# Kernel optimization log

Hardware: AMD Instinct MI355X
Metric: run time of the kernel (lower is better)

## Reference

```python
import jax, jax.numpy as jnp
import numpy as np

D_MODEL = 1024
N_HEAD = 16
D_K = D_MODEL // N_HEAD
NEG = -1000000000.0


def setup_inputs() -> dict:
    key = jax.random.key(0)
    ks = jax.random.split(key, 12)
    B, S = 4, 2048
    scale = 1.0 / np.sqrt(D_MODEL)
    inp = {
        "q": jax.random.normal(ks[0], (B, S, D_MODEL), jnp.float32),
        "k": jax.random.normal(ks[1], (B, S, D_MODEL), jnp.float32),
        "v": jax.random.normal(ks[2], (B, S, D_MODEL), jnp.float32),
        "mask": jnp.ones((1, 1, S, S), jnp.int32),
        "w_Q": jax.random.normal(ks[3], (D_MODEL, D_MODEL), jnp.float32) * scale,
        "b_Q": jnp.zeros((D_MODEL,), jnp.float32),
        "w_K": jax.random.normal(ks[4], (D_MODEL, D_MODEL), jnp.float32) * scale,
        "b_K": jnp.zeros((D_MODEL,), jnp.float32),
        "w_V": jax.random.normal(ks[5], (D_MODEL, D_MODEL), jnp.float32) * scale,
        "b_V": jnp.zeros((D_MODEL,), jnp.float32),
        "w_O": jax.random.normal(ks[6], (D_MODEL, D_MODEL), jnp.float32) * scale,
        "b_O": jnp.zeros((D_MODEL,), jnp.float32),
    }
    return inp


def reference(q, k, v, mask, w_Q, b_Q, w_K, b_K, w_V, b_V, w_O, b_O):
    B, S, _ = q.shape
    # linear projections (torch Linear: x @ W^T + b)
    qp = q @ w_Q.T + b_Q
    kp = k @ w_K.T + b_K
    vp = v @ w_V.T + b_V
    # [B,S,D] -> [B,H,S,d_k]
    qh = qp.reshape(B, S, N_HEAD, D_K).transpose(0, 2, 1, 3)
    kh = kp.reshape(B, S, N_HEAD, D_K).transpose(0, 2, 1, 3)
    vh = vp.reshape(B, S, N_HEAD, D_K).transpose(0, 2, 1, 3)
    # scores [B,H,S,S]
    scores = jnp.einsum("bhqd,bhkd->bhqk", qh, kh) / jnp.sqrt(jnp.float32(D_K))
    scores = jnp.where(mask == 0, jnp.float32(NEG), scores)
    attn = jax.nn.softmax(scores, axis=-1)  # dropout p=0.0 -> identity
    ctx = jnp.einsum("bhqk,bhkd->bhqd", attn, vh)
    ctx = ctx.transpose(0, 2, 1, 3).reshape(B, S, D_MODEL)
    return ctx @ w_O.T + b_O
```

## Files before the change

### kernel.cpp

```cpp
#include <hip/hip_runtime.h>
#include <hip/hip_bf16.h>
#include <cmath>

#define D_MODEL 1024
#define N_HEAD 16
#define D_K 64

typedef __attribute__((ext_vector_type(8))) short short8;
typedef __attribute__((ext_vector_type(4))) float f32x4;
typedef __attribute__((ext_vector_type(16))) float f32x16;

#define GL_LDS16(gp, lp)                                                                   \
  __builtin_amdgcn_global_load_lds((const __attribute__((address_space(1))) unsigned int*)(gp), \
                                   (__attribute__((address_space(3))) unsigned int*)(lp), 16, 0, 0)

#if __has_builtin(__builtin_amdgcn_exp2f)
#define EXP2(x) __builtin_amdgcn_exp2f(x)
#else
#define EXP2(x) exp2f(x)
#endif

__device__ __forceinline__ unsigned short f2bu(float x) {
  __hip_bfloat16 h = __float2bfloat16(x);
  return *reinterpret_cast<unsigned short*>(&h);
}

__device__ __forceinline__ unsigned int cvtpk(float lo, float hi) {
  unsigned int r;
  asm("v_cvt_pk_bf16_f32 %0, %1, %2" : "=v"(r) : "v"(lo), "v"(hi));
  return r;
}

__device__ __forceinline__ float max3f(float a, float b, float c) {
  return fmaxf(fmaxf(a, b), c);
}

__device__ __forceinline__ void plswap(unsigned int& a, unsigned int& b) {
#if __has_builtin(__builtin_amdgcn_permlane32_swap)
  auto r = __builtin_amdgcn_permlane32_swap((int)a, (int)b, false, false);
  a = (unsigned int)r[0];
  b = (unsigned int)r[1];
#else
  unsigned int ax = (unsigned int)__shfl_xor((int)a, 32);
  unsigned int bx = (unsigned int)__shfl_xor((int)b, 32);
  bool hi = (threadIdx.x & 32) != 0;
  unsigned int na = hi ? bx : a;
  unsigned int nb = hi ? b : ax;
  a = na; b = nb;
#endif
}

__global__ __launch_bounds__(256) void f2b3_kernel(const float* __restrict__ a, const float* __restrict__ b,
                                                   const float* __restrict__ c,
                                                   unsigned short* __restrict__ oa, unsigned short* __restrict__ ob,
                                                   unsigned short* __restrict__ oc, int n) {
  const float* src = (blockIdx.y == 0) ? a : (blockIdx.y == 1) ? b : c;
  unsigned short* dst = (blockIdx.y == 0) ? oa : (blockIdx.y == 1) ? ob : oc;
  int i = (blockIdx.x * 256 + threadIdx.x) * 4;
  if (i >= n) return;
  float4 v = *reinterpret_cast<const float4*>(src + i);
  ushort4 o;
  o.x = f2bu(v.x); o.y = f2bu(v.y); o.z = f2bu(v.z); o.w = f2bu(v.w);
  *reinterpret_cast<ushort4*>(dst + i) = o;
}

__global__ __launch_bounds__(256) void f2b4_kernel(const float* __restrict__ a, const float* __restrict__ b,
                                                   const float* __restrict__ c, const float* __restrict__ d,
                                                   unsigned short* __restrict__ oa, unsigned short* __restrict__ ob,
                                                   unsigned short* __restrict__ oc, unsigned short* __restrict__ od,
                                                   int n) {
  const float* src = (blockIdx.y == 0) ? a : (blockIdx.y == 1) ? b : (blockIdx.y == 2) ? c : d;
  unsigned short* dst = (blockIdx.y == 0) ? oa : (blockIdx.y == 1) ? ob : (blockIdx.y == 2) ? oc : od;
  int i = (blockIdx.x * 256 + threadIdx.x) * 4;
  if (i >= n) return;
  float4 v = *reinterpret_cast<const float4*>(src + i);
  ushort4 o;
  o.x = f2bu(v.x); o.y = f2bu(v.y); o.z = f2bu(v.z); o.w = f2bu(v.w);
  *reinterpret_cast<ushort4*>(dst + i) = o;
}

template <int OUTF32>
__global__ __launch_bounds__(256) void gemm_bt_kernel(
    const unsigned short* __restrict__ A0, const unsigned short* __restrict__ A1,
    const unsigned short* __restrict__ A2,
    const unsigned short* __restrict__ W0, const unsigned short* __restrict__ W1,
    const unsigned short* __restrict__ W2,
    const float* __restrict__ b0, const float* __restrict__ b1, const float* __restrict__ b2,
    void* __restrict__ Cout, int Msub, int N, int K,
    float s0, float s1, float s2) {
  __shared__ __align__(16) unsigned short lA[2][128 * 64];
  __shared__ __align__(16) unsigned short lB[2][128 * 64];

  const int tid = threadIdx.x;
  const int lane = tid & 63;
  const int w = tid >> 6;
  const int wm = w >> 1, wn = w & 1;
  const int lr = lane & 15, lg = lane >> 4;
  const int wavebase = tid & ~63;

  int m0g, n0;
  {
    const int nbx = gridDim.x;
    const int nb = nbx * gridDim.y;
    int lin = blockIdx.y * nbx + blockIdx.x;
    int wid = lin;
    if ((nb & 7) == 0) wid = (lin & 7) * (nb >> 3) + (lin >> 3);
    n0 = (wid % nbx) * 128;
    m0g = (wid / nbx) * 128;
  }
  const int mtile = m0g >> 7;
  const int which = mtile / (Msub >> 7);
  const int m0 = m0g - which * Msub;
  const unsigned short* A  = (which == 0) ? A0 : (which == 1) ? A1 : A2;
  const unsigned short* Bw = (which == 0) ? W0 : (which == 1) ? W1 : W2;
  const float* bias = (which == 0) ? b0 : (which == 1) ? b1 : b2;
  const float oscale = (which == 0) ? s0 : (which == 1) ? s1 : s2;

  f32x4 acc[4][4] = {};

  auto stage = [&](int buf, int k0) {
#pragma unroll
    for (int j = 0; j < 4; ++j) {
      int chunk = j * 256 + tid;
      int row = chunk >> 3, cc = chunk & 7;
      GL_LDS16(A + (size_t)(m0 + row) * K + k0 + cc * 8,
               (char*)&lA[buf][0] + (j * 256 + wavebase) * 16);
    }
#pragma unroll
    for (int j = 0; j < 4; ++j) {
      int chunk = j * 256 + tid;
      int row = chunk >> 3, cc = chunk & 7;
      GL_LDS16(Bw + (size_t)(n0 + row) * K + k0 + cc * 8,
               (char*)&lB[buf][0] + (j * 256 + wavebase) * 16);
    }
  };

  stage(0, 0);
  const int nk = K / 64;
  for (int t = 0; t < nk; ++t) {
    const int buf = t & 1;
    __syncthreads();
    if (t + 1 < nk) stage(buf ^ 1, (t + 1) * 64);
#pragma unroll
    for (int kk = 0; kk < 2; ++kk) {
      short8 a[4], bfr[4];
#pragma unroll
      for (int m = 0; m < 4; ++m)
        a[m] = *reinterpret_cast<const short8*>(
            &lA[buf][(wm * 64 + m * 16 + lr) * 64 + kk * 32 + lg * 8]);
#pragma unroll
      for (int n = 0; n < 4; ++n)
        bfr[n] = *reinterpret_cast<const short8*>(
            &lB[buf][(wn * 64 + n * 16 + lr) * 64 + kk * 32 + lg * 8]);
#pragma unroll
      for (int m = 0; m < 4; ++m)
#pragma unroll
        for (int n = 0; n < 4; ++n)
          acc[m][n] = __builtin_amdgcn_mfma_f32_16x16x32_bf16(a[m], bfr[n], acc[m][n], 0, 0, 0);
    }
  }

#pragma unroll
  for (int n = 0; n < 4; ++n) {
    const int gc = n0 + wn * 64 + n * 16 + lr;
    const float bn = bias[gc];
#pragma unroll
    for (int m = 0; m < 4; ++m) {
      const int gr0 = m0g + wm * 64 + m * 16 + lg * 4;
#pragma unroll
      for (int i = 0; i < 4; ++i) {
        float v = (acc[m][n][i] + bn) * oscale;
        if (OUTF32)
          reinterpret_cast<float*>(Cout)[(size_t)(gr0 + i) * N + gc] = v;
        else
          reinterpret_cast<unsigned short*>(Cout)[(size_t)(gr0 + i) * N + gc] = f2bu(v);
      }
    }
  }
}

__global__ __launch_bounds__(512, 4) void attn_kernel(
    const unsigned short* __restrict__ Qp, const unsigned short* __restrict__ Kp,
    const unsigned short* __restrict__ Vp, unsigned short* __restrict__ Ctx, int S) {
  __shared__ __align__(16) unsigned short Ks[2][64 * 64];
  __shared__ __align__(16) unsigned short Vt[2][64 * 64];

  const int tid = threadIdx.x;
  const int lane = tid & 63;
  const int wv = tid >> 6;
  const int l31 = lane & 31;
  const int hf = lane >> 5;

  const int nqb = gridDim.x;
  const int total = nqb * gridDim.y;
  int f = blockIdx.y * nqb + blockIdx.x;
  int g = ((total & 7) == 0) ? ((f & 7) * (total >> 3) + (f >> 3)) : f;
  const int bh = g / nqb;
  const int b = bh >> 4;
  const int head = bh & 15;
  const int q0 = (g % nqb) * 256;
  const int qrow = q0 + wv * 32 + l31;

  int av[4], av2[4];
#pragma unroll
  for (int c = 0; c < 4; ++c) {
    int chunk = ((c * 2 + hf) ^ (l31 & 7) ^ (l31 >> 3)) & 7;
    av[c] = l31 * 128 + (chunk << 4);
    av2[c] = (av[c] ^ 0x40) + 4096;
  }

  const unsigned short* qptr = Qp + (size_t)(b * S + qrow) * D_MODEL + head * 64;
  short8 qf[4];
#pragma unroll
  for (int ds = 0; ds < 4; ++ds)
    qf[ds] = *reinterpret_cast<const short8*>(qptr + ds * 16 + hf * 8);

  const int t256 = tid & 255;
  const int dblk = t256 & 15, kblk = t256 >> 4;
  const int dv0 = dblk * 4, key0 = kblk * 4;
  int wbyte[4];
#pragma unroll
  for (int j = 0; j < 4; ++j) {
    int row = dv0 + j;
    int slot = ((key0 >> 3) ^ (row & 7) ^ ((row >> 3) & 7)) & 7;
    wbyte[j] = row * 128 + (slot << 4) + ((key0 & 4) << 1);
  }

  float m_run = -1e30f, l_run = 0.0f;
  f32x16 oacc0 = {}, oacc1 = {};

  auto stageK = [&](int buf, int t) {
    const size_t baseK = (size_t)(b * S + t * 64) * D_MODEL + head * 64;
#pragma unroll
    for (int j = 0; j < 2; ++j) {
      int c = j * 256 + t256;
      int r = c >> 3, w8 = c & 7;
      int w8s = w8 ^ (r & 7) ^ ((r >> 3) & 7);
      GL_LDS16(Kp + baseK + (size_t)r * D_MODEL + w8s * 8,
               (char*)&Ks[buf][0] + (j * 256 + (t256 & ~63)) * 16);
    }
  };

  uint2 vr0, vr1, vr2, vr3;
  auto loadV = [&](int t) {
    const unsigned short* vptr =
        Vp + (size_t)(b * S + t * 64 + key0) * D_MODEL + head * 64 + dv0;
    vr0 = *reinterpret_cast<const uint2*>(vptr);
    vr1 = *reinterpret_cast<const uint2*>(vptr + D_MODEL);
    vr2 = *reinterpret_cast<const uint2*>(vptr + 2 * D_MODEL);
    vr3 = *reinterpret_cast<const uint2*>(vptr + 3 * D_MODEL);
  };

  if (wv >= 4) stageK(0, 0);
  else loadV(0);

  const int nt = S / 64;
  auto tile = [&](const int buf, const int t) {
    if (wv < 4) {
      char* vb = (char*)&Vt[buf][0];
      unsigned int o0x = __builtin_amdgcn_perm(vr1.x, vr0.x, 0x05040100u);
      unsigned int o0y = __builtin_amdgcn_perm(vr3.x, vr2.x, 0x05040100u);
      unsigned int o1x = __builtin_amdgcn_perm(vr1.x, vr0.x, 0x07060302u);
      unsigned int o1y = __builtin_amdgcn_perm(vr3.x, vr2.x, 0x07060302u);
      unsigned int o2x = __builtin_amdgcn_perm(vr1.y, vr0.y, 0x05040100u);
      unsigned int o2y = __builtin_amdgcn_perm(vr3.y, vr2.y, 0x05040100u);
      unsigned int o3x = __builtin_amdgcn_perm(vr1.y, vr0.y, 0x07060302u);
      unsigned int o3y = __builtin_amdgcn_perm(vr3.y, vr2.y, 0x07060302u);
      *reinterpret_cast<uint2*>(vb + wbyte[0]) = make_uint2(o0x, o0y);
      *reinterpret_cast<uint2*>(vb + wbyte[1]) = make_uint2(o1x, o1y);
      *reinterpret_cast<uint2*>(vb + wbyte[2]) = make_uint2(o2x, o2y);
      *reinterpret_cast<uint2*>(vb + wbyte[3]) = make_uint2(o3x, o3y);
    }
    __syncthreads();
    if (t + 1 < nt) {
      if (wv >= 4) stageK(buf ^ 1, t + 1);
      else loadV(t + 1);
    }

    const char* kbp = (const char*)&Ks[buf][0];
    const char* vbp = (const char*)&Vt[buf][0];

#pragma unroll
    for (int h2 = 0; h2 < 2; ++h2) {
      f32x16 sacc = {};
      __builtin_amdgcn_s_setprio(1);
#pragma unroll
      for (int ds = 0; ds < 4; ++ds) {
        short8 a0 = *reinterpret_cast<const short8*>(kbp + (h2 ? av2[ds] : av[ds]));
        sacc = __builtin_amdgcn_mfma_f32_32x32x16_bf16(a0, qf[ds], sacc, 0, 0, 0);
      }
      __builtin_amdgcn_s_setprio(0);

      float a0 = max3f(sacc[0], sacc[1], sacc[2]);
      float a1 = max3f(sacc[3], sacc[4], sacc[5]);
      float a2 = max3f(sacc[6], sacc[7], sacc[8]);
      float a3 = max3f(sacc[9], sacc[10], sacc[11]);
      float a4 = max3f(sacc[12], sacc[13], sacc[14]);
      float b0 = max3f(a0, a1, sacc[15]);
      float b1 = max3f(a2, a3, a4);
      float rmax_h = fmaxf(b0, b1);
      float rmax = fmaxf(rmax_h, __shfl_xor(rmax_h, 32));

      if (__any(rmax > m_run + 8.0f)) {
        float mnew = fmaxf(m_run, rmax);
        float al = EXP2(m_run - mnew);
        m_run = mnew;
        l_run *= al;
#pragma unroll
        for (int r = 0; r < 16; ++r) { oacc0[r] *= al; oacc1[r] *= al; }
      }

#pragma unroll
      for (int r = 0; r < 16; ++r) sacc[r] = EXP2(sacc[r] - m_run);

      float s0 = (sacc[0] + sacc[1]) + (sacc[2] + sacc[3]);
      float s1 = (sacc[4] + sacc[5]) + (sacc[6] + sacc[7]);
      float s2 = (sacc[8] + sacc[9]) + (sacc[10] + sacc[11]);
      float s3 = (sacc[12] + sacc[13]) + (sacc[14] + sacc[15]);
      float rsum = (s0 + s1) + (s2 + s3);
      rsum += __shfl_xor(rsum, 32);
      l_run += rsum;

      unsigned int W[8];
#pragma unroll
      for (int m = 0; m < 8; ++m) W[m] = cvtpk(sacc[2 * m], sacc[2 * m + 1]);
      short8 pf[2];
#pragma unroll
      for (int s = 0; s < 2; ++s) {
        unsigned int u0 = W[4 * s + 0], u2 = W[4 * s + 2];
        unsigned int u1 = W[4 * s + 1], u3 = W[4 * s + 3];
        plswap(u0, u2); plswap(u1, u3);
        int4 wvv = make_int4((int)u0, (int)u1, (int)u2, (int)u3);
        pf[s] = *reinterpret_cast<short8*>(&wvv);
      }

      __builtin_amdgcn_s_setprio(1);
#pragma unroll
      for (int s = 0; s < 2; ++s) {
        short8 va = *reinterpret_cast<const short8*>(vbp + av[h2 * 2 + s]);
        oacc0 = __builtin_amdgcn_mfma_f32_32x32x16_bf16(va, pf[s], oacc0, 0, 0, 0);
        short8 vb2 = *reinterpret_cast<const short8*>(vbp + av2[h2 * 2 + s]);
        oacc1 = __builtin_amdgcn_mfma_f32_32x32x16_bf16(vb2, pf[s], oacc1, 0, 0, 0);
      }
      __builtin_amdgcn_s_setprio(0);
    }
  };

  for (int t = 0; t < nt; t += 2) {
    tile(0, t);
    tile(1, t + 1);
  }

  const float linv = 1.0f / l_run;
  unsigned short* cp = Ctx + (size_t)(b * S + qrow) * D_MODEL + head * 64;
#pragma unroll
  for (int g2 = 0; g2 < 4; ++g2) {
    ushort4 o;
    o.x = f2bu(oacc0[4 * g2 + 0] * linv);
    o.y = f2bu(oacc0[4 * g2 + 1] * linv);
    o.z = f2bu(oacc0[4 * g2 + 2] * linv);
    o.w = f2bu(oacc0[4 * g2 + 3] * linv);
    *reinterpret_cast<ushort4*>(cp + 8 * g2 + 4 * hf) = o;
    ushort4 o2;
    o2.x = f2bu(oacc1[4 * g2 + 0] * linv);
    o2.y = f2bu(oacc1[4 * g2 + 1] * linv);
    o2.z = f2bu(oacc1[4 * g2 + 2] * linv);
    o2.w = f2bu(oacc1[4 * g2 + 3] * linv);
    *reinterpret_cast<ushort4*>(cp + 32 + 8 * g2 + 4 * hf) = o2;
  }
}

extern "C" void kernel_launch(void* const* d_in, const int* in_sizes, int n_in,
                              void* d_out, int out_size, void* d_ws, size_t ws_size,
                              hipStream_t stream) {
  const float* q  = (const float*)d_in[0];
  const float* k  = (const float*)d_in[1];
  const float* v  = (const float*)d_in[2];
  const float* wQ = (const float*)d_in[4];
  const float* bQ = (const float*)d_in[5];
  const float* wK = (const float*)d_in[6];
  const float* bK = (const float*)d_in[7];
  const float* wV = (const float*)d_in[8];
  const float* bV = (const float*)d_in[9];
  const float* wO = (const float*)d_in[10];
  const float* bO = (const float*)d_in[11];
  float* out = (float*)d_out;

  int S = 1;
  while ((long)S * S < (long)in_sizes[3]) S <<= 1;
  const int Bn = in_sizes[0] / (S * D_MODEL);
  const int M = Bn * S;

  unsigned short* xq   = (unsigned short*)d_ws;
  unsigned short* wqb  = xq + (size_t)M * D_MODEL;
  unsigned short* wkb  = wqb + (size_t)D_MODEL * D_MODEL;
  unsigned short* wvb  = wkb + (size_t)D_MODEL * D_MODEL;
  unsigned short* wob  = wvb + (size_t)D_MODEL * D_MODEL;
  unsigned short* qkvp = wob + (size_t)D_MODEL * D_MODEL;
  unsigned short* qp = qkvp;
  unsigned short* kp = qkvp + (size_t)M * D_MODEL;
  unsigned short* vp = qkvp + 2 * (size_t)M * D_MODEL;
  unsigned short* xk = (unsigned short*)d_out;
  unsigned short* xv = xk + (size_t)M * D_MODEL;

  const int DW = D_MODEL * D_MODEL;
  f2b4_kernel<<<dim3(DW / 1024, 4), 256, 0, stream>>>(wQ, wK, wV, wO, wqb, wkb, wvb, wob, DW);

  const int NX = M * D_MODEL;
  f2b3_kernel<<<dim3(NX / 1024, 3), 256, 0, stream>>>(q, k, v, xq, xk, xv, NX);

  const float qscale = 0.125f * 1.4426950408889634f;

  gemm_bt_kernel<0><<<dim3(D_MODEL / 128, 3 * M / 128), 256, 0, stream>>>(
      xq, xk, xv, wqb, wkb, wvb, bQ, bK, bV, qkvp, M, D_MODEL, D_MODEL,
      qscale, 1.0f, 1.0f);

  attn_kernel<<<dim3(S / 256, Bn * N_HEAD), 512, 0, stream>>>(qp, kp, vp, xq, S);

  gemm_bt_kernel<1><<<dim3(D_MODEL / 128, M / 128), 256, 0, stream>>>(
      xq, xq, xq, wob, wob, wob, bO, bO, bO, out, M, D_MODEL, D_MODEL,
      1.0f, 1.0f, 1.0f);
}
```

Before: 222.1 us.

## Triple-buffer projection GEMM with swizzled LDS and explicit vmcnt waits

The projection GEMM moves from a double-buffered K=64 tile to a triple-buffered K=32 tile. LDS chunks are XOR-swizzled to avoid bank conflicts on the MFMA fragment reads. Explicit s_waitcnt vmcnt counts and raw barriers let up to two future stages stay in flight, and s_setprio is raised around the MFMA block. This aims to hide global-to-LDS latency and cut LDS conflicts, at the cost of more barriers per K step and hand-tuned wait counts that must match the number of loads issued per stage.

```diff
diff --git a/kernel.cpp b/kernel.cpp
--- a/kernel.cpp
+++ b/kernel.cpp
@@ -88,8 +88,8 @@
     const float* __restrict__ b0, const float* __restrict__ b1, const float* __restrict__ b2,
     void* __restrict__ Cout, int Msub, int N, int K,
     float s0, float s1, float s2) {
-  __shared__ __align__(16) unsigned short lA[2][128 * 64];
-  __shared__ __align__(16) unsigned short lB[2][128 * 64];
+  __shared__ __align__(16) unsigned short lA[3][128 * 32];
+  __shared__ __align__(16) unsigned short lB[3][128 * 32];
 
   const int tid = threadIdx.x;
   const int lane = tid & 63;
@@ -118,46 +118,66 @@
 
   f32x4 acc[4][4] = {};
 
+  const int swz = (lg ^ (lr & 3) ^ ((lr >> 2) & 3)) << 4;
+  int avA[4], avB[4];
+#pragma unroll
+  for (int m = 0; m < 4; ++m) {
+    avA[m] = (wm * 64 + m * 16 + lr) * 64 + swz;
+    avB[m] = (wn * 64 + m * 16 + lr) * 64 + swz;
+  }
+
   auto stage = [&](int buf, int k0) {
 #pragma unroll
-    for (int j = 0; j < 4; ++j) {
-      int chunk = j * 256 + tid;
-      int row = chunk >> 3, cc = chunk & 7;
-      GL_LDS16(A + (size_t)(m0 + row) * K + k0 + cc * 8,
+    for (int j = 0; j < 2; ++j) {
+      int c = j * 256 + tid;
+      int row = c >> 2, cc = c & 3;
+      int gc = (cc ^ (row & 3) ^ ((row >> 2) & 3)) * 8;
+      GL_LDS16(A + (size_t)(m0 + row) * K + k0 + gc,
                (char*)&lA[buf][0] + (j * 256 + wavebase) * 16);
     }
 #pragma unroll
-    for (int j = 0; j < 4; ++j) {
-      int chunk = j * 256 + tid;
-      int row = chunk >> 3, cc = chunk & 7;
-      GL_LDS16(Bw + (size_t)(n0 + row) * K + k0 + cc * 8,
+    for (int j = 0; j < 2; ++j) {
+      int c = j * 256 + tid;
+      int row = c >> 2, cc = c & 3;
+      int gc = (cc ^ (row & 3) ^ ((row >> 2) & 3)) * 8;
+      GL_LDS16(Bw + (size_t)(n0 + row) * K + k0 + gc,
                (char*)&lB[buf][0] + (j * 256 + wavebase) * 16);
     }
   };
 
+  const int nk = K / 32;
   stage(0, 0);
-  const int nk = K / 64;
+  stage(1, 32);
+  stage(2, 64);
+
+  int buf = 0;
   for (int t = 0; t < nk; ++t) {
-    const int buf = t & 1;
-    __syncthreads();
-    if (t + 1 < nk) stage(buf ^ 1, (t + 1) * 64);
-#pragma unroll
-    for (int kk = 0; kk < 2; ++kk) {
-      short8 a[4], bfr[4];
-#pragma unroll
-      for (int m = 0; m < 4; ++m)
-        a[m] = *reinterpret_cast<const short8*>(
-            &lA[buf][(wm * 64 + m * 16 + lr) * 64 + kk * 32 + lg * 8]);
+    if (t < nk - 2)       asm volatile("s_waitcnt vmcnt(8)" ::: "memory");
+    else if (t == nk - 2) asm volatile("s_waitcnt vmcnt(4)" ::: "memory");
+    else                  asm volatile("s_waitcnt vmcnt(0)" ::: "memory");
+    __builtin_amdgcn_s_barrier();
+    __builtin_amdgcn_sched_barrier(0);
+
+    const char* pA = (const char*)&lA[buf][0];
+    const char* pB = (const char*)&lB[buf][0];
+    short8 a[4], bb[4];
+#pragma unroll
+    for (int m = 0; m < 4; ++m) a[m] = *reinterpret_cast<const short8*>(pA + avA[m]);
+#pragma unroll
+    for (int n = 0; n < 4; ++n) bb[n] = *reinterpret_cast<const short8*>(pB + avB[n]);
+
+    __builtin_amdgcn_s_setprio(1);
+#pragma unroll
+    for (int m = 0; m < 4; ++m)
 #pragma unroll
       for (int n = 0; n < 4; ++n)
-        bfr[n] = *reinterpret_cast<const short8*>(
-            &lB[buf][(wn * 64 + n * 16 + lr) * 64 + kk * 32 + lg * 8]);
-#pragma unroll
-      for (int m = 0; m < 4; ++m)
-#pragma unroll
-        for (int n = 0; n < 4; ++n)
-          acc[m][n] = __builtin_amdgcn_mfma_f32_16x16x32_bf16(a[m], bfr[n], acc[m][n], 0, 0, 0);
-    }
+        acc[m][n] = __builtin_amdgcn_mfma_f32_16x16x32_bf16(a[m], bb[n], acc[m][n], 0, 0, 0);
+    __builtin_amdgcn_s_setprio(0);
+
+    __builtin_amdgcn_s_barrier();
+    __builtin_amdgcn_sched_barrier(0);
+    if (t + 3 < nk) stage(buf, (t + 3) * 32);
+    buf = (buf == 2) ? 0 : buf + 1;
   }
 
 #pragma unroll
```

Result: faster. 204.6 us (-7.9%).
